# Performance work log

Hardware: AMD Instinct MI355X
Metric: run time of the kernel (lower is better)

## Reference

```python
import jax, jax.numpy as jnp
import numpy as np

EPS_NORM = 1e-12
BN_EPS = 1e-5
TEMP = 0.07


def _l2norm(x, axis):
    n = jnp.sqrt(jnp.sum(x * x, axis=axis, keepdims=True))
    return x / jnp.maximum(n, EPS_NORM)


def _bn_eval(z, w, b):
    # inference-mode BatchNorm2d with running_mean=0, running_var=1
    s = w / jnp.sqrt(jnp.asarray(1.0 + BN_EPS, z.dtype))
    return z * s[None, :, None, None] + b[None, :, None, None]


def setup_inputs() -> dict:
    key = jax.random.key(0)
    ks = jax.random.split(key, 8)
    B, C, H, W = 16, 256, 64, 64
    KD, P = 128, 256
    x = jax.random.normal(ks[0], (B, C, H, W), jnp.float32)
    m_features = jax.random.normal(ks[1], (P, KD), jnp.float32)
    q_w = jax.random.normal(ks[2], (KD, C), jnp.float32) * 0.05
    k_w = jax.random.normal(ks[3], (KD, KD), jnp.float32) * 0.05
    v_w = jax.random.normal(ks[4], (KD, KD), jnp.float32) * 0.05
    o_w = jax.random.normal(ks[5], (C, KD), jnp.float32) * 0.05
    dw_w = jax.random.normal(ks[6], (C, 1, 3, 3), jnp.float32) * 0.1
    return {
        "x": x, "m_features": m_features,
        "q_w": q_w, "q_b": jnp.zeros((KD,), jnp.float32),
        "k_w": k_w, "k_b": jnp.zeros((KD,), jnp.float32),
        "v_w": v_w, "v_b": jnp.zeros((KD,), jnp.float32),
        "o_w": o_w, "o_b": jnp.zeros((C,), jnp.float32),
        "dw_w": dw_w,
        "bn1_w": jnp.ones((C,), jnp.float32), "bn1_b": jnp.zeros((C,), jnp.float32),
        "bn2_w": jnp.ones((C,), jnp.float32), "bn2_b": jnp.zeros((C,), jnp.float32),
        "gamma": jnp.ones((C,), jnp.float32) * 1e-5,
    }


def reference(x, m_features, q_w, q_b, k_w, k_b, v_w, v_b, o_w, o_b,
              dw_w, bn1_w, bn1_b, bn2_w, bn2_b, gamma):
    B, C, H, W = x.shape
    KD = q_w.shape[0]
    residual = x
    # q_proj 1x1 conv -> [B,KD,H,W], L2-normalize over channel dim
    q = jnp.einsum('bchw,kc->bkhw', x, q_w) + q_b[None, :, None, None]
    q = _l2norm(q, axis=1)
    q = q.reshape(B, KD, H * W).transpose(0, 2, 1)  # [B, HW, KD]
    # k/v projections of memory bank [P, KD]
    k = _l2norm(m_features @ k_w.T + k_b, axis=-1)
    v = m_features @ v_w.T + v_b
    # fp32 attention with clamped logits
    q32, k32, v32 = q.astype(jnp.float32), k.astype(jnp.float32), v.astype(jnp.float32)
    logits = jnp.clip(jnp.einsum('bnd,pd->bnp', q32, k32) / TEMP, -30.0, 30.0)
    attn = jax.nn.softmax(logits, axis=-1)
    out = jnp.einsum('bnp,pd->bnd', attn, v32).astype(x.dtype)
    out = out.transpose(0, 2, 1).reshape(B, KD, H, W)
    # out_proj 1x1 conv -> [B,C,H,W]
    out = jnp.einsum('bkhw,ck->bchw', out, o_w) + o_b[None, :, None, None]
    # local branch: depthwise 3x3 conv + BN + exact GELU
    local = jax.lax.conv_general_dilated(
        out, dw_w, window_strides=(1, 1), padding='SAME',
        feature_group_count=C,
        dimension_numbers=('NCHW', 'OIHW', 'NCHW'))
    local = jax.nn.gelu(_bn_eval(local, bn1_w, bn1_b), approximate=False)
    out = out + local
    return _bn_eval(residual + out * gamma[None, :, None, None], bn2_w, bn2_b)
```

## Files before the change

### kernel.cpp

```cpp
#include <hip/hip_runtime.h>
#include <hip/hip_bf16.h>
#include <math.h>

#define B_ 16
#define C_ 256
#define H_ 64
#define W_ 64
#define KD_ 128
#define P_ 256
#define HW_ (H_ * W_)

typedef __bf16 bf16;
typedef bf16 bf16x8_t __attribute__((ext_vector_type(8)));
typedef float f32x4_t __attribute__((ext_vector_type(4)));
typedef float f32x16_t __attribute__((ext_vector_type(16)));
typedef unsigned char u8;

__device__ __forceinline__ unsigned cvt_pk_fp8_lo(float a, float b, unsigned old) {
#if __has_builtin(__builtin_amdgcn_cvt_pk_fp8_f32)
    return __builtin_amdgcn_cvt_pk_fp8_f32(a, b, old, false);
#else
    unsigned r = old;
    asm("v_cvt_pk_fp8_f32 %0, %1, %2" : "+v"(r) : "v"(a), "v"(b));
    return r;
#endif
}
__device__ __forceinline__ unsigned cvt_pk_fp8_hi(float a, float b, unsigned old) {
#if __has_builtin(__builtin_amdgcn_cvt_pk_fp8_f32)
    return __builtin_amdgcn_cvt_pk_fp8_f32(a, b, old, true);
#else
    unsigned r = old;
    asm("v_cvt_pk_fp8_f32 %0, %1, %2 op_sel:[0,0,1]" : "+v"(r) : "v"(a), "v"(b));
    return r;
#endif
}
__device__ __forceinline__ uint2 pack8_fp8(const float* f) {
    uint2 r;
    r.x = cvt_pk_fp8_hi(f[2], f[3], cvt_pk_fp8_lo(f[0], f[1], 0u));
    r.y = cvt_pk_fp8_hi(f[6], f[7], cvt_pk_fp8_lo(f[4], f[5], 0u));
    return r;
}

__global__ __launch_bounds__(128) void k_prep1(
    const float* __restrict__ m_feat,
    const float* __restrict__ k_w, const float* __restrict__ k_b,
    const float* __restrict__ v_w, const float* __restrict__ v_b,
    float* __restrict__ kn_f, float* __restrict__ v_f)
{
    const int p = blockIdx.x;
    const int j = threadIdx.x;
    __shared__ float msh[KD_];
    __shared__ float red[2];
    msh[j] = m_feat[p * KD_ + j];
    __syncthreads();

    float ka = k_b[j];
    float va = v_b[j];
#pragma unroll 4
    for (int d = 0; d < KD_; ++d) {
        const float m = msh[d];
        ka = fmaf(m, k_w[j * KD_ + d], ka);
        va = fmaf(m, v_w[j * KD_ + d], va);
    }
    float s = ka * ka;
#pragma unroll
    for (int o = 1; o < 64; o <<= 1) s += __shfl_xor(s, o);
    if ((j & 63) == 0) red[j >> 6] = s;
    __syncthreads();
    s = red[0] + red[1];
    const float inv = 1.0f / (0.07f * fmaxf(sqrtf(s), 1e-12f));
    kn_f[p * KD_ + j] = ka * inv;
    v_f[p * KD_ + j] = va;
}

__global__ __launch_bounds__(256) void k_prep23(
    const float* __restrict__ o_w, const float* __restrict__ v_f,
    const float* __restrict__ q_w, const float* __restrict__ kn_f,
    u8* __restrict__ m28, u8* __restrict__ qw8, u8* __restrict__ kn8)
{
    if (blockIdx.x < 256) {
        const int c = blockIdx.x;
        const int p = threadIdx.x;
        __shared__ float osh[KD_];
        if (p < KD_) osh[p] = o_w[c * KD_ + p];
        __syncthreads();
        float acc = 0.f;
#pragma unroll 4
        for (int k = 0; k < KD_; ++k) acc = fmaf(osh[k], v_f[p * KD_ + k], acc);
        const int mt = c >> 5, r = c & 31;
        const int ks = p >> 4, sub = (p >> 3) & 1, jj = p & 7;
        const unsigned pk = cvt_pk_fp8_lo(acc * 16.0f, 0.f, 0u);
        m28[(((mt * 16 + ks) * 64) + sub * 32 + r) * 8 + jj] = (u8)(pk & 0xffu);
    } else {
        const int t = (blockIdx.x - 256) * 256 + threadIdx.x;
        float f[8];
        if (t < 4096) {
            const int lane = t & 63, g = t >> 6, mt = g >> 4, ks = g & 15;
            const int row = mt * 32 + (lane & 31), k0 = ks * 16 + (lane >> 5) * 8;
            const float* src = q_w + row * C_ + k0;
#pragma unroll
            for (int j = 0; j < 8; ++j) f[j] = src[j] * 16.0f;
            ((uint2*)qw8)[t] = pack8_fp8(f);
        } else {
            const int u = t - 4096;
            const int lane = u & 63, g = u >> 6, mt = g >> 3, ks = g & 7;
            const int row = mt * 32 + (lane & 31), k0 = ks * 16 + (lane >> 5) * 8;
            const float* src = kn_f + row * KD_ + k0;
#pragma unroll
            for (int j = 0; j < 8; ++j) f[j] = src[j];
            ((uint2*)kn8)[u] = pack8_fp8(f);
        }
    }
}

__global__ __launch_bounds__(256, 4) void k_attn(
    const float* __restrict__ x,
    const float* __restrict__ q_b, const float* __restrict__ o_b,
    const u8* __restrict__ qw8, const u8* __restrict__ kn8,
    const u8* __restrict__ m28, bf16* __restrict__ outf)
{
    __shared__ __align__(16) char lds[27648];
    char* const xs   = lds;
    char* const qbuf = lds + 16384;
    char* const ebuf = lds;
    float* ss_lds   = (float*)(lds + 24576);
    float* pmax_lds = (float*)(lds + 25600);
    float* sum_lds  = (float*)(lds + 26624);

    const int h = blockIdx.x;
    const int b = blockIdx.y;
    const int tid = threadIdx.x;
    const int lane = tid & 63;
    const int wid = tid >> 6;
    const int l31 = lane & 31;
    const int kh  = lane >> 5;

    {
        const int wq = tid & 15;
        const int cg = tid >> 4;
        const float* xrow = x + (size_t)b * C_ * HW_ + h * W_;
#pragma unroll
        for (int half = 0; half < 2; ++half) {
            const int c0 = cg * 16 + half * 8;
            float v[8][4];
#pragma unroll
            for (int jj = 0; jj < 8; ++jj) {
                const f32x4_t t = *(const f32x4_t*)(xrow + (size_t)(c0 + jj) * HW_ + wq * 4);
                v[jj][0] = t[0]; v[jj][1] = t[1]; v[jj][2] = t[2]; v[jj][3] = t[3];
            }
#pragma unroll
            for (int k = 0; k < 4; ++k) {
                const int pix = wq * 4 + k;
                float f[8];
#pragma unroll
                for (int jj = 0; jj < 8; ++jj) f[jj] = v[jj][k];
                *(uint2*)(xs + pix * 256 + (c0 ^ ((pix & 31) << 3))) = pack8_fp8(f);
            }
        }
    }
    __syncthreads();

    f32x16_t qacc[2];
#pragma unroll
    for (int nt = 0; nt < 2; ++nt)
#pragma unroll
        for (int i = 0; i < 16; ++i) qacc[nt][i] = 0.f;
#pragma unroll
    for (int ks = 0; ks < 16; ++ks) {
        const long a = *(const long*)(qw8 + ((wid * 16 + ks) * 64 + lane) * 8);
#pragma unroll
        for (int nt = 0; nt < 2; ++nt) {
            const int pix = nt * 32 + l31;
            const long bx = *(const long*)(xs + pix * 256 + ((ks * 16 + kh * 8) ^ (l31 << 3)));
            qacc[nt] = __builtin_amdgcn_mfma_f32_32x32x16_fp8_fp8(a, bx, qacc[nt], 0, 0, 0);
        }
    }
    {
        f32x4_t qbv[4];
#pragma unroll
        for (int g = 0; g < 4; ++g)
            qbv[g] = *(const f32x4_t*)(q_b + wid * 32 + g * 8 + kh * 4);
#pragma unroll
        for (int nt = 0; nt < 2; ++nt) {
            const int pix = nt * 32 + l31;
            float ssp = 0.f;
#pragma unroll
            for (int reg = 0; reg < 16; ++reg) {
                const int g = reg >> 2, i = reg & 3;
                const float qv = qacc[nt][reg] + 16.0f * qbv[g][i];
                qacc[nt][reg] = qv;
                ssp = fmaf(qv, qv, ssp);
            }
            ssp += __shfl_xor(ssp, 32);
            if (lane < 32) ss_lds[pix * 4 + wid] = ssp;
#pragma unroll
            for (int g = 0; g < 4; ++g) {
                const unsigned qw_ = cvt_pk_fp8_hi(qacc[nt][g * 4 + 2], qacc[nt][g * 4 + 3],
                                    cvt_pk_fp8_lo(qacc[nt][g * 4 + 0], qacc[nt][g * 4 + 1], 0u));
                *(unsigned*)(qbuf + pix * 128 +
                             ((wid * 32 + g * 8 + kh * 4) ^ ((l31 & 15) << 3))) = qw_;
            }
        }
    }
    __syncthreads();

    f32x16_t lacc[2][2];
#pragma unroll
    for (int m = 0; m < 2; ++m)
#pragma unroll
        for (int nt = 0; nt < 2; ++nt)
#pragma unroll
            for (int i = 0; i < 16; ++i) lacc[m][nt][i] = 0.f;
#pragma unroll
    for (int ks = 0; ks < 8; ++ks) {
        const long a0 = *(const long*)(kn8 + (((wid * 2 + 0) * 8 + ks) * 64 + lane) * 8);
        const long a1 = *(const long*)(kn8 + (((wid * 2 + 1) * 8 + ks) * 64 + lane) * 8);
#pragma unroll
        for (int nt = 0; nt < 2; ++nt) {
            const int pix = nt * 32 + l31;
            const long bq = *(const long*)(qbuf + pix * 128 +
                                           ((ks * 16 + kh * 8) ^ ((l31 & 15) << 3)));
            lacc[0][nt] = __builtin_amdgcn_mfma_f32_32x32x16_fp8_fp8(a0, bq, lacc[0][nt], 0, 0, 0);
            lacc[1][nt] = __builtin_amdgcn_mfma_f32_32x32x16_fp8_fp8(a1, bq, lacc[1][nt], 0, 0, 0);
        }
    }
#pragma unroll
    for (int nt = 0; nt < 2; ++nt) {
        const int pix = nt * 32 + l31;
        float mx = lacc[0][nt][0];
#pragma unroll
        for (int i = 1; i < 16; ++i) mx = fmaxf(mx, lacc[0][nt][i]);
#pragma unroll
        for (int i = 0; i < 16; ++i) mx = fmaxf(mx, lacc[1][nt][i]);
        mx = fmaxf(mx, __shfl_xor(mx, 32));
        if (lane < 32) pmax_lds[pix * 4 + wid] = mx;
    }
    __syncthreads();

#pragma unroll
    for (int nt = 0; nt < 2; ++nt) {
        const int pix = nt * 32 + l31;
        const f32x4_t s4 = *(const f32x4_t*)(ss_lds + pix * 4);
        const float qinv = 1.0f / fmaxf(sqrtf(s4[0] + s4[1] + s4[2] + s4[3]), 1e-12f);
        const f32x4_t m4 = *(const f32x4_t*)(pmax_lds + pix * 4);
        const float cof = 5.545177444479562f -
                          fmaxf(fmaxf(m4[0], m4[1]), fmaxf(m4[2], m4[3])) * qinv;
        float sm = 0.f;
#pragma unroll
        for (int m = 0; m < 2; ++m) {
#pragma unroll
            for (int g = 0; g < 4; ++g) {
                float e[4];
#pragma unroll
                for (int i = 0; i < 4; ++i) {
                    e[i] = __expf(fmaf(lacc[m][nt][g * 4 + i], qinv, cof));
                    sm += e[i];
                }
                const unsigned ew = cvt_pk_fp8_hi(e[2], e[3],
                                    cvt_pk_fp8_lo(e[0], e[1], 0u));
                const int p0 = (wid * 2 + m) * 32 + g * 8 + kh * 4;
                *(unsigned*)(ebuf + pix * 256 + (p0 ^ (l31 << 3))) = ew;
            }
        }
        sm += __shfl_xor(sm, 32);
        if (lane < 32) sum_lds[pix * 4 + wid] = sm;
    }
    __syncthreads();

    f32x16_t oacc[2][2];
#pragma unroll
    for (int m = 0; m < 2; ++m)
#pragma unroll
        for (int nt = 0; nt < 2; ++nt)
#pragma unroll
            for (int i = 0; i < 16; ++i) oacc[m][nt][i] = 0.f;
#pragma unroll
    for (int ks = 0; ks < 16; ++ks) {
        const long a0 = *(const long*)(m28 + (((wid * 2 + 0) * 16 + ks) * 64 + lane) * 8);
        const long a1 = *(const long*)(m28 + (((wid * 2 + 1) * 16 + ks) * 64 + lane) * 8);
#pragma unroll
        for (int nt = 0; nt < 2; ++nt) {
            const int pix = nt * 32 + l31;
            const long be = *(const long*)(ebuf + pix * 256 +
                                           ((ks * 16 + kh * 8) ^ (l31 << 3)));
            oacc[0][nt] = __builtin_amdgcn_mfma_f32_32x32x16_fp8_fp8(a0, be, oacc[0][nt], 0, 0, 0);
            oacc[1][nt] = __builtin_amdgcn_mfma_f32_32x32x16_fp8_fp8(a1, be, oacc[1][nt], 0, 0, 0);
        }
    }
    {
        bf16* const obase = outf + (size_t)b * C_ * HW_ + h * W_;
#pragma unroll
        for (int m = 0; m < 2; ++m) {
            const int cw = (wid * 2 + m) * 32;
            f32x4_t obv[4];
#pragma unroll
            for (int g = 0; g < 4; ++g)
                obv[g] = *(const f32x4_t*)(o_b + cw + g * 8 + kh * 4);
#pragma unroll
            for (int nt = 0; nt < 2; ++nt) {
                const int pix = nt * 32 + l31;
                const f32x4_t sv = *(const f32x4_t*)(sum_lds + pix * 4);
                const float rs = 1.0f / (16.0f * (sv[0] + sv[1] + sv[2] + sv[3]));
#pragma unroll
                for (int reg = 0; reg < 16; ++reg) {
                    const int g = reg >> 2, i = reg & 3;
                    const int c = cw + g * 8 + kh * 4 + i;
                    obase[(size_t)c * HW_ + pix] = (bf16)fmaf(oacc[m][nt][reg], rs, obv[g][i]);
                }
            }
        }
    }
}

__global__ __launch_bounds__(256) void k_post(
    const float* __restrict__ x, const bf16* __restrict__ outf,
    const float* __restrict__ dw_w,
    const float* __restrict__ bn1_w, const float* __restrict__ bn1_b,
    const float* __restrict__ bn2_w, const float* __restrict__ bn2_b,
    const float* __restrict__ gamma, float* __restrict__ y)
{
    __shared__ __align__(16) bf16 os[HW_];
    const int bc = blockIdx.x;
    const int c = bc & (C_ - 1);
    const int tid = threadIdx.x;

    const bf16* oc = outf + (size_t)bc * HW_;
#pragma unroll
    for (int it = 0; it < 2; ++it) {
        const int e = (it * 256 + tid) * 8;
        *(bf16x8_t*)&os[e] = *(const bf16x8_t*)&oc[e];
    }

    const float cbn = 0.99999500003750f;
    const float s1 = bn1_w[c] * cbn, b1 = bn1_b[c];
    const float s2 = bn2_w[c] * cbn, b2 = bn2_b[c];
    const float g = gamma[c];
    float kw[9];
#pragma unroll
    for (int j = 0; j < 9; ++j) kw[j] = dw_w[c * 9 + j];

    __syncthreads();

    const int w = tid & 63;
    const int h0 = (tid >> 6) * 16;

    float r0[3], r1[3], r2[3];
    auto ldrow = [&](int hh, float* r) {
        if ((unsigned)hh < (unsigned)H_) {
            r[1] = (float)os[hh * W_ + w];
            r[0] = (w > 0) ? (float)os[hh * W_ + w - 1] : 0.f;
            r[2] = (w < W_ - 1) ? (float)os[hh * W_ + w + 1] : 0.f;
        } else {
            r[0] = r[1] = r[2] = 0.f;
        }
    };
    ldrow(h0 - 1, r0);
    ldrow(h0, r1);

    const float* xc = x + (size_t)bc * HW_;
    float* yc = y + (size_t)bc * HW_;

#pragma unroll
    for (int i = 0; i < 16; ++i) {
        const int h = h0 + i;
        ldrow(h + 1, r2);
        float conv = kw[0] * r0[0];
        conv = fmaf(kw[1], r0[1], conv);
        conv = fmaf(kw[2], r0[2], conv);
        conv = fmaf(kw[3], r1[0], conv);
        conv = fmaf(kw[4], r1[1], conv);
        conv = fmaf(kw[5], r1[2], conv);
        conv = fmaf(kw[6], r2[0], conv);
        conv = fmaf(kw[7], r2[1], conv);
        conv = fmaf(kw[8], r2[2], conv);
        const float center = r1[1];
        const float t = fmaf(conv, s1, b1);
        const float lg = t / (1.0f + __expf(-1.702f * t));
        const int idx = h * W_ + w;
        yc[idx] = fmaf(center + lg, g, xc[idx]) * s2 + b2;
#pragma unroll
        for (int j = 0; j < 3; ++j) { r0[j] = r1[j]; r1[j] = r2[j]; }
    }
}

extern "C" void kernel_launch(void* const* d_in, const int* in_sizes, int n_in,
                              void* d_out, int out_size, void* d_ws, size_t ws_size,
                              hipStream_t stream)
{
    const float* x     = (const float*)d_in[0];
    const float* m_f   = (const float*)d_in[1];
    const float* q_w   = (const float*)d_in[2];
    const float* q_b   = (const float*)d_in[3];
    const float* k_w   = (const float*)d_in[4];
    const float* k_b   = (const float*)d_in[5];
    const float* v_w   = (const float*)d_in[6];
    const float* v_b   = (const float*)d_in[7];
    const float* o_w   = (const float*)d_in[8];
    const float* o_b   = (const float*)d_in[9];
    const float* dw_w  = (const float*)d_in[10];
    const float* bn1_w = (const float*)d_in[11];
    const float* bn1_b = (const float*)d_in[12];
    const float* bn2_w = (const float*)d_in[13];
    const float* bn2_b = (const float*)d_in[14];
    const float* gamma = (const float*)d_in[15];

    char* ws = (char*)d_ws;
    u8*    qw8   = (u8*)(ws);
    u8*    kn8   = (u8*)(ws + (32 << 10));
    u8*    m28   = (u8*)(ws + (64 << 10));
    bf16*  outf  = (bf16*)(ws + (384 << 10));
    float* kn_f  = (float*)(ws + (384 << 10));
    float* v_f   = (float*)(ws + (384 << 10) + (128 << 10));

    k_prep1<<<dim3(P_), dim3(128), 0, stream>>>(m_f, k_w, k_b, v_w, v_b,
                                                kn_f, v_f);
    k_prep23<<<dim3(288), dim3(256), 0, stream>>>(o_w, v_f, q_w, kn_f,
                                                  m28, qw8, kn8);
    k_attn<<<dim3(H_, B_), dim3(256), 0, stream>>>(x, q_b, o_b, qw8, kn8,
                                                   m28, outf);
    k_post<<<dim3(B_ * C_), dim3(256), 0, stream>>>(
        x, outf, dw_w, bn1_w, bn1_b, bn2_w, bn2_b, gamma, (float*)d_out);
}
```

Before: 74.94 us.

## Split attention row into two 32-pixel halves to cut registers and LDS

The attention kernel now processes each 64-pixel row as two sequential 32-pixel tiles instead of both tiles at once. This halves the live MFMA accumulators and shrinks shared memory from 27.6KB to 22KB, which could allow more resident blocks. It also loads x for both halves up front and converts the second half into LDS while the first half's logits are computed, overlapping staging with compute. The cost is more barriers, each weight fragment (qw8, kn8, m28) being loaded twice, and less MFMA work per weight load.

```diff
diff --git a/kernel.cpp b/kernel.cpp
--- a/kernel.cpp
+++ b/kernel.cpp
@@ -119,13 +119,11 @@
     const u8* __restrict__ qw8, const u8* __restrict__ kn8,
     const u8* __restrict__ m28, bf16* __restrict__ outf)
 {
-    __shared__ __align__(16) char lds[27648];
-    char* const xs   = lds;
+    __shared__ __align__(16) char lds[22016];
     char* const qbuf = lds + 16384;
-    char* const ebuf = lds;
-    float* ss_lds   = (float*)(lds + 24576);
-    float* pmax_lds = (float*)(lds + 25600);
-    float* sum_lds  = (float*)(lds + 26624);
+    float* const ss_lds   = (float*)(lds + 20480);
+    float* const pmax_lds = (float*)(lds + 20992);
+    float* const sum_lds  = (float*)(lds + 21504);
 
     const int h = blockIdx.x;
     const int b = blockIdx.y;
@@ -135,177 +133,158 @@
     const int l31 = lane & 31;
     const int kh  = lane >> 5;
 
-    {
-        const int wq = tid & 15;
-        const int cg = tid >> 4;
-        const float* xrow = x + (size_t)b * C_ * HW_ + h * W_;
-#pragma unroll
-        for (int half = 0; half < 2; ++half) {
-            const int c0 = cg * 16 + half * 8;
-            float v[8][4];
-#pragma unroll
-            for (int jj = 0; jj < 8; ++jj) {
-                const f32x4_t t = *(const f32x4_t*)(xrow + (size_t)(c0 + jj) * HW_ + wq * 4);
-                v[jj][0] = t[0]; v[jj][1] = t[1]; v[jj][2] = t[2]; v[jj][3] = t[3];
+    const int wq = tid & 7;
+    const int cg = tid >> 3;
+    const int c0 = cg * 8;
+    const float* xrow = x + (size_t)b * C_ * HW_ + h * W_ + wq * 4;
+    float v0[8][4], v1[8][4];
+#pragma unroll
+    for (int jj = 0; jj < 8; ++jj) {
+        const f32x4_t t0 = *(const f32x4_t*)(xrow + (size_t)(c0 + jj) * HW_);
+        v0[jj][0] = t0[0]; v0[jj][1] = t0[1]; v0[jj][2] = t0[2]; v0[jj][3] = t0[3];
+    }
+#pragma unroll
+    for (int jj = 0; jj < 8; ++jj) {
+        const f32x4_t t1 = *(const f32x4_t*)(xrow + (size_t)(c0 + jj) * HW_ + 32);
+        v1[jj][0] = t1[0]; v1[jj][1] = t1[1]; v1[jj][2] = t1[2]; v1[jj][3] = t1[3];
+    }
+#pragma unroll
+    for (int k = 0; k < 4; ++k) {
+        const int pix = wq * 4 + k;
+        float f[8];
+#pragma unroll
+        for (int jj = 0; jj < 8; ++jj) f[jj] = v0[jj][k];
+        *(uint2*)(lds + pix * 256 + (c0 ^ (pix << 3))) = pack8_fp8(f);
+    }
+    __syncthreads();
+
+#pragma unroll
+    for (int t = 0; t < 2; ++t) {
+        char* const xe = lds + t * 8192;
+
+        f32x16_t qacc;
+#pragma unroll
+        for (int i = 0; i < 16; ++i) qacc[i] = 0.f;
+#pragma unroll
+        for (int ks = 0; ks < 16; ++ks) {
+            const long a = *(const long*)(qw8 + ((wid * 16 + ks) * 64 + lane) * 8);
+            const long bx = *(const long*)(xe + l31 * 256 + ((ks * 16 + kh * 8) ^ (l31 << 3)));
+            qacc = __builtin_amdgcn_mfma_f32_32x32x16_fp8_fp8(a, bx, qacc, 0, 0, 0);
+        }
+        {
+            float ssp = 0.f;
+#pragma unroll
+            for (int g = 0; g < 4; ++g) {
+                const f32x4_t qbv = *(const f32x4_t*)(q_b + wid * 32 + g * 8 + kh * 4);
+#pragma unroll
+                for (int i = 0; i < 4; ++i) {
+                    const float qv = qacc[g * 4 + i] + 16.0f * qbv[i];
+                    qacc[g * 4 + i] = qv;
+                    ssp = fmaf(qv, qv, ssp);
+                }
             }
+            ssp += __shfl_xor(ssp, 32);
+            if (lane < 32) ss_lds[l31 * 4 + wid] = ssp;
+#pragma unroll
+            for (int g = 0; g < 4; ++g) {
+                const unsigned qw_ = cvt_pk_fp8_hi(qacc[g * 4 + 2], qacc[g * 4 + 3],
+                                    cvt_pk_fp8_lo(qacc[g * 4 + 0], qacc[g * 4 + 1], 0u));
+                *(unsigned*)(qbuf + l31 * 128 +
+                             ((wid * 32 + g * 8 + kh * 4) ^ ((l31 & 15) << 3))) = qw_;
+            }
+        }
+        __syncthreads();
+
+        f32x16_t lacc0, lacc1;
+#pragma unroll
+        for (int i = 0; i < 16; ++i) { lacc0[i] = 0.f; lacc1[i] = 0.f; }
+#pragma unroll
+        for (int ks = 0; ks < 8; ++ks) {
+            const long a0 = *(const long*)(kn8 + (((wid * 2 + 0) * 8 + ks) * 64 + lane) * 8);
+            const long a1 = *(const long*)(kn8 + (((wid * 2 + 1) * 8 + ks) * 64 + lane) * 8);
+            const long bq = *(const long*)(qbuf + l31 * 128 +
+                                           ((ks * 16 + kh * 8) ^ ((l31 & 15) << 3)));
+            lacc0 = __builtin_amdgcn_mfma_f32_32x32x16_fp8_fp8(a0, bq, lacc0, 0, 0, 0);
+            lacc1 = __builtin_amdgcn_mfma_f32_32x32x16_fp8_fp8(a1, bq, lacc1, 0, 0, 0);
+        }
+        {
+            float mx = lacc0[0];
+#pragma unroll
+            for (int i = 1; i < 16; ++i) mx = fmaxf(mx, lacc0[i]);
+#pragma unroll
+            for (int i = 0; i < 16; ++i) mx = fmaxf(mx, lacc1[i]);
+            mx = fmaxf(mx, __shfl_xor(mx, 32));
+            if (lane < 32) pmax_lds[l31 * 4 + wid] = mx;
+        }
+        if (t == 0) {
 #pragma unroll
             for (int k = 0; k < 4; ++k) {
                 const int pix = wq * 4 + k;
                 float f[8];
 #pragma unroll
-                for (int jj = 0; jj < 8; ++jj) f[jj] = v[jj][k];
-                *(uint2*)(xs + pix * 256 + (c0 ^ ((pix & 31) << 3))) = pack8_fp8(f);
+                for (int jj = 0; jj < 8; ++jj) f[jj] = v1[jj][k];
+                *(uint2*)(lds + 8192 + pix * 256 + (c0 ^ (pix << 3))) = pack8_fp8(f);
             }
         }
-    }
-    __syncthreads();
-
-    f32x16_t qacc[2];
-#pragma unroll
-    for (int nt = 0; nt < 2; ++nt)
-#pragma unroll
-        for (int i = 0; i < 16; ++i) qacc[nt][i] = 0.f;
-#pragma unroll
-    for (int ks = 0; ks < 16; ++ks) {
-        const long a = *(const long*)(qw8 + ((wid * 16 + ks) * 64 + lane) * 8);
-#pragma unroll
-        for (int nt = 0; nt < 2; ++nt) {
-            const int pix = nt * 32 + l31;
-            const long bx = *(const long*)(xs + pix * 256 + ((ks * 16 + kh * 8) ^ (l31 << 3)));
-            qacc[nt] = __builtin_amdgcn_mfma_f32_32x32x16_fp8_fp8(a, bx, qacc[nt], 0, 0, 0);
-        }
-    }
-    {
-        f32x4_t qbv[4];
-#pragma unroll
-        for (int g = 0; g < 4; ++g)
-            qbv[g] = *(const f32x4_t*)(q_b + wid * 32 + g * 8 + kh * 4);
-#pragma unroll
-        for (int nt = 0; nt < 2; ++nt) {
-            const int pix = nt * 32 + l31;
-            float ssp = 0.f;
-#pragma unroll
-            for (int reg = 0; reg < 16; ++reg) {
-                const int g = reg >> 2, i = reg & 3;
-                const float qv = qacc[nt][reg] + 16.0f * qbv[g][i];
-                qacc[nt][reg] = qv;
-                ssp = fmaf(qv, qv, ssp);
+        __syncthreads();
+
+        {
+            const f32x4_t s4 = *(const f32x4_t*)(ss_lds + l31 * 4);
+            const float qinv = 1.0f / fmaxf(sqrtf(s4[0] + s4[1] + s4[2] + s4[3]), 1e-12f);
+            const f32x4_t m4 = *(const f32x4_t*)(pmax_lds + l31 * 4);
+            const float cof = 5.545177444479562f -
+                              fmaxf(fmaxf(m4[0], m4[1]), fmaxf(m4[2], m4[3])) * qinv;
+            float sm = 0.f;
+#pragma unroll
+            for (int m = 0; m < 2; ++m) {
+#pragma unroll
+                for (int g = 0; g < 4; ++g) {
+                    float e[4];
+#pragma unroll
+                    for (int i = 0; i < 4; ++i) {
+                        const float lv = (m == 0) ? lacc0[g * 4 + i] : lacc1[g * 4 + i];
+                        e[i] = __expf(fmaf(lv, qinv, cof));
+                        sm += e[i];
+                    }
+                    const unsigned ew = cvt_pk_fp8_hi(e[2], e[3],
+                                        cvt_pk_fp8_lo(e[0], e[1], 0u));
+                    const int p0 = (wid * 2 + m) * 32 + g * 8 + kh * 4;
+                    *(unsigned*)(xe + l31 * 256 + (p0 ^ (l31 << 3))) = ew;
+                }
             }
-            ssp += __shfl_xor(ssp, 32);
-            if (lane < 32) ss_lds[pix * 4 + wid] = ssp;
-#pragma unroll
-            for (int g = 0; g < 4; ++g) {
-                const unsigned qw_ = cvt_pk_fp8_hi(qacc[nt][g * 4 + 2], qacc[nt][g * 4 + 3],
-                                    cvt_pk_fp8_lo(qacc[nt][g * 4 + 0], qacc[nt][g * 4 + 1], 0u));
-                *(unsigned*)(qbuf + pix * 128 +
-                             ((wid * 32 + g * 8 + kh * 4) ^ ((l31 & 15) << 3))) = qw_;
-            }
-        }
-    }
-    __syncthreads();
-
-    f32x16_t lacc[2][2];
-#pragma unroll
-    for (int m = 0; m < 2; ++m)
-#pragma unroll
-        for (int nt = 0; nt < 2; ++nt)
-#pragma unroll
-            for (int i = 0; i < 16; ++i) lacc[m][nt][i] = 0.f;
-#pragma unroll
-    for (int ks = 0; ks < 8; ++ks) {
-        const long a0 = *(const long*)(kn8 + (((wid * 2 + 0) * 8 + ks) * 64 + lane) * 8);
-        const long a1 = *(const long*)(kn8 + (((wid * 2 + 1) * 8 + ks) * 64 + lane) * 8);
-#pragma unroll
-        for (int nt = 0; nt < 2; ++nt) {
-            const int pix = nt * 32 + l31;
-            const long bq = *(const long*)(qbuf + pix * 128 +
-                                           ((ks * 16 + kh * 8) ^ ((l31 & 15) << 3)));
-            lacc[0][nt] = __builtin_amdgcn_mfma_f32_32x32x16_fp8_fp8(a0, bq, lacc[0][nt], 0, 0, 0);
-            lacc[1][nt] = __builtin_amdgcn_mfma_f32_32x32x16_fp8_fp8(a1, bq, lacc[1][nt], 0, 0, 0);
-        }
-    }
-#pragma unroll
-    for (int nt = 0; nt < 2; ++nt) {
-        const int pix = nt * 32 + l31;
-        float mx = lacc[0][nt][0];
-#pragma unroll
-        for (int i = 1; i < 16; ++i) mx = fmaxf(mx, lacc[0][nt][i]);
-#pragma unroll
-        for (int i = 0; i < 16; ++i) mx = fmaxf(mx, lacc[1][nt][i]);
-        mx = fmaxf(mx, __shfl_xor(mx, 32));
-        if (lane < 32) pmax_lds[pix * 4 + wid] = mx;
-    }
-    __syncthreads();
-
-#pragma unroll
-    for (int nt = 0; nt < 2; ++nt) {
-        const int pix = nt * 32 + l31;
-        const f32x4_t s4 = *(const f32x4_t*)(ss_lds + pix * 4);
-        const float qinv = 1.0f / fmaxf(sqrtf(s4[0] + s4[1] + s4[2] + s4[3]), 1e-12f);
-        const f32x4_t m4 = *(const f32x4_t*)(pmax_lds + pix * 4);
-        const float cof = 5.545177444479562f -
-                          fmaxf(fmaxf(m4[0], m4[1]), fmaxf(m4[2], m4[3])) * qinv;
-        float sm = 0.f;
-#pragma unroll
-        for (int m = 0; m < 2; ++m) {
-#pragma unroll
-            for (int g = 0; g < 4; ++g) {
-                float e[4];
-#pragma unroll
-                for (int i = 0; i < 4; ++i) {
-                    e[i] = __expf(fmaf(lacc[m][nt][g * 4 + i], qinv, cof));
-                    sm += e[i];
-                }
-                const unsigned ew = cvt_pk_fp8_hi(e[2], e[3],
-                                    cvt_pk_fp8_lo(e[0], e[1], 0u));
-                const int p0 = (wid * 2 + m) * 32 + g * 8 + kh * 4;
-                *(unsigned*)(ebuf + pix * 256 + (p0 ^ (l31 << 3))) = ew;
-            }
-        }
-        sm += __shfl_xor(sm, 32);
-        if (lane < 32) sum_lds[pix * 4 + wid] = sm;
-    }
-    __syncthreads();
-
-    f32x16_t oacc[2][2];
-#pragma unroll
-    for (int m = 0; m < 2; ++m)
-#pragma unroll
-        for (int nt = 0; nt < 2; ++nt)
-#pragma unroll
-            for (int i = 0; i < 16; ++i) oacc[m][nt][i] = 0.f;
-#pragma unroll
-    for (int ks = 0; ks < 16; ++ks) {
-        const long a0 = *(const long*)(m28 + (((wid * 2 + 0) * 16 + ks) * 64 + lane) * 8);
-        const long a1 = *(const long*)(m28 + (((wid * 2 + 1) * 16 + ks) * 64 + lane) * 8);
-#pragma unroll
-        for (int nt = 0; nt < 2; ++nt) {
-            const int pix = nt * 32 + l31;
-            const long be = *(const long*)(ebuf + pix * 256 +
+            sm += __shfl_xor(sm, 32);
+            if (lane < 32) sum_lds[l31 * 4 + wid] = sm;
+        }
+        __syncthreads();
+
+        f32x16_t oacc0, oacc1;
+#pragma unroll
+        for (int i = 0; i < 16; ++i) { oacc0[i] = 0.f; oacc1[i] = 0.f; }
+#pragma unroll
+        for (int ks = 0; ks < 16; ++ks) {
+            const long a0 = *(const long*)(m28 + (((wid * 2 + 0) * 16 + ks) * 64 + lane) * 8);
+            const long a1 = *(const long*)(m28 + (((wid * 2 + 1) * 16 + ks) * 64 + lane) * 8);
+            const long be = *(const long*)(xe + l31 * 256 +
                                            ((ks * 16 + kh * 8) ^ (l31 << 3)));
-            oacc[0][nt] = __builtin_amdgcn_mfma_f32_32x32x16_fp8_fp8(a0, be, oacc[0][nt], 0, 0, 0);
-            oacc[1][nt] = __builtin_amdgcn_mfma_f32_32x32x16_fp8_fp8(a1, be, oacc[1][nt], 0, 0, 0);
-        }
-    }
-    {
-        bf16* const obase = outf + (size_t)b * C_ * HW_ + h * W_;
-#pragma unroll
-        for (int m = 0; m < 2; ++m) {
-            const int cw = (wid * 2 + m) * 32;
-            f32x4_t obv[4];
-#pragma unroll
-            for (int g = 0; g < 4; ++g)
-                obv[g] = *(const f32x4_t*)(o_b + cw + g * 8 + kh * 4);
-#pragma unroll
-            for (int nt = 0; nt < 2; ++nt) {
-                const int pix = nt * 32 + l31;
-                const f32x4_t sv = *(const f32x4_t*)(sum_lds + pix * 4);
-                const float rs = 1.0f / (16.0f * (sv[0] + sv[1] + sv[2] + sv[3]));
-#pragma unroll
-                for (int reg = 0; reg < 16; ++reg) {
-                    const int g = reg >> 2, i = reg & 3;
-                    const int c = cw + g * 8 + kh * 4 + i;
-                    obase[(size_t)c * HW_ + pix] = (bf16)fmaf(oacc[m][nt][reg], rs, obv[g][i]);
+            oacc0 = __builtin_amdgcn_mfma_f32_32x32x16_fp8_fp8(a0, be, oacc0, 0, 0, 0);
+            oacc1 = __builtin_amdgcn_mfma_f32_32x32x16_fp8_fp8(a1, be, oacc1, 0, 0, 0);
+        }
+        {
+            const f32x4_t sv = *(const f32x4_t*)(sum_lds + l31 * 4);
+            const float rs = 1.0f / (16.0f * (sv[0] + sv[1] + sv[2] + sv[3]));
+            bf16* const obase = outf + (size_t)b * C_ * HW_ + h * W_ + t * 32 + l31;
+#pragma unroll
+            for (int m = 0; m < 2; ++m) {
+                const int cw = (wid * 2 + m) * 32;
+#pragma unroll
+                for (int g = 0; g < 4; ++g) {
+                    const f32x4_t obv = *(const f32x4_t*)(o_b + cw + g * 8 + kh * 4);
+#pragma unroll
+                    for (int i = 0; i < 4; ++i) {
+                        const float ov = (m == 0) ? oacc0[g * 4 + i] : oacc1[g * 4 + i];
+                        const int c = cw + g * 8 + kh * 4 + i;
+                        obase[(size_t)c * HW_] = (bf16)fmaf(ov, rs, obv[i]);
+                    }
                 }
             }
         }
```

New measurement: 102.4 us. 1.37x slower.
